# Performance work log

Measured on AMD Instinct MI355X. Metric: run time of the kernel, lower is better.

Reference implementation:

```python
import jax, jax.numpy as jnp
import numpy as np

B, S, D, H = 2, 2048, 1024, 16
DK = D // H


def setup_inputs() -> dict:
    key = jax.random.key(0)
    ks = jax.random.split(key, 12)
    scale = 1.0 / np.sqrt(D)
    return {
        "query": jax.random.normal(ks[0], (B, S, D), jnp.float32),
        "key": jax.random.normal(ks[1], (B, S, D), jnp.float32),
        "value": jax.random.normal(ks[2], (B, S, D), jnp.float32),
        "mask": jax.random.randint(ks[3], (B, S), 0, 2, jnp.int32),
        "Wq": jax.random.normal(ks[4], (D, D), jnp.float32) * scale,
        "bq": jnp.zeros((D,), jnp.float32),
        "Wk": jax.random.normal(ks[5], (D, D), jnp.float32) * scale,
        "bk": jnp.zeros((D,), jnp.float32),
        "Wv": jax.random.normal(ks[6], (D, D), jnp.float32) * scale,
        "bv": jnp.zeros((D,), jnp.float32),
        "Wo": jax.random.normal(ks[7], (D, D), jnp.float32) * scale,
        "bo": jnp.zeros((D,), jnp.float32),
    }


def _proj_split(x, W, b):
    # torch Linear: x @ W.T + b, then [B,S,D] -> [B,H,S,DK]
    y = x @ W.T + b
    return y.reshape(B, S, H, DK).transpose(0, 2, 1, 3)


def reference(query, key, value, mask, Wq, bq, Wk, bk, Wv, bv, Wo, bo):
    q = _proj_split(query, Wq, bq)  # [B,H,S,DK]
    k = _proj_split(key, Wk, bk)
    v = _proj_split(value, Wv, bv)
    scores = jnp.einsum("bhqd,bhkd->bhqk", q, k) / jnp.sqrt(jnp.float32(DK))
    # 2D mask -> [B,1,1,S], masked_fill(mask==0, -1e9)
    m = mask[:, None, None, :]
    scores = jnp.where(m == 0, jnp.float32(-1e9), scores)
    attn = jax.nn.softmax(scores, axis=-1)  # dropout p=0.0 -> identity
    x = jnp.einsum("bhqk,bhkd->bhqd", attn, v)
    x = x.transpose(0, 2, 1, 3).reshape(B, S, D)
    output = x @ Wo.T + bo
    return output, attn
```

## Files before the change

kernel.cpp:

```cpp
#include <hip/hip_runtime.h>
#include <hip/hip_bf16.h>
#include <stdint.h>

typedef __bf16 bf16;
typedef __bf16 bf16x8 __attribute__((ext_vector_type(8)));
typedef float f32x4 __attribute__((ext_vector_type(4)));

#define MFMA16(a, b, c) __builtin_amdgcn_mfma_f32_16x16x32_bf16((a), (b), (c), 0, 0, 0)

__device__ __forceinline__ void g2lds16(const void* g, void* l) {
  __builtin_amdgcn_global_load_lds((__attribute__((address_space(1))) void*)g,
                                   (__attribute__((address_space(3))) void*)l,
                                   16, 0, 0);
}

__global__ __launch_bounds__(256) void cvt3(const float* __restrict__ a,
                                            const float* __restrict__ b,
                                            const float* __restrict__ c,
                                            bf16* x, bf16* y, bf16* z_) {
  int zi = blockIdx.y;
  const float* s = (zi == 0) ? a : (zi == 1) ? b : c;
  bf16* d = (zi == 0) ? x : (zi == 1) ? y : z_;
  size_t i = ((size_t)blockIdx.x * 256 + threadIdx.x) * 8;
  float4 f0 = *(const float4*)(s + i);
  float4 f1 = *(const float4*)(s + i + 4);
  union { bf16 h[8]; uint4 u; } t;
  t.h[0] = (bf16)f0.x; t.h[1] = (bf16)f0.y; t.h[2] = (bf16)f0.z; t.h[3] = (bf16)f0.w;
  t.h[4] = (bf16)f1.x; t.h[5] = (bf16)f1.y; t.h[6] = (bf16)f1.z; t.h[7] = (bf16)f1.w;
  *(uint4*)(d + i) = t.u;
}
__global__ __launch_bounds__(256) void cvt4(const float* __restrict__ a,
                                            const float* __restrict__ b,
                                            const float* __restrict__ c,
                                            const float* __restrict__ e,
                                            bf16* x, bf16* y, bf16* z_, bf16* w) {
  int zi = blockIdx.y;
  const float* s = (zi == 0) ? a : (zi == 1) ? b : (zi == 2) ? c : e;
  bf16* d = (zi == 0) ? x : (zi == 1) ? y : (zi == 2) ? z_ : w;
  size_t i = ((size_t)blockIdx.x * 256 + threadIdx.x) * 8;
  float4 f0 = *(const float4*)(s + i);
  float4 f1 = *(const float4*)(s + i + 4);
  union { bf16 h[8]; uint4 u; } t;
  t.h[0] = (bf16)f0.x; t.h[1] = (bf16)f0.y; t.h[2] = (bf16)f0.z; t.h[3] = (bf16)f0.w;
  t.h[4] = (bf16)f1.x; t.h[5] = (bf16)f1.y; t.h[6] = (bf16)f1.z; t.h[7] = (bf16)f1.w;
  *(uint4*)(d + i) = t.u;
}

__device__ __forceinline__ void gemm_core_128(const bf16* __restrict__ A,
                                              const bf16* __restrict__ W,
                                              int m0, int n0, int tid,
                                              uint4* sA, uint4* sB,
                                              f32x4 acc[4][4]) {
  const int lane = tid & 63, quad = lane >> 4, l16 = lane & 15;
  const int wave = tid >> 6;
  const int wm = (wave >> 1) * 64, wn = (wave & 1) * 64;
#pragma unroll
  for (int i = 0; i < 4; i++)
#pragma unroll
    for (int j = 0; j < 4; j++) {
      f32x4 z = {0.f, 0.f, 0.f, 0.f};
      acc[i][j] = z;
    }
  for (int kk = 0; kk < 16; kk++) {
    const int k0 = kk * 64;
    __syncthreads();
#pragma unroll
    for (int t = 0; t < 4; t++) {
      int c = t * 256 + tid;
      int r = c >> 3, jb = (c & 7) ^ (r & 7);
      g2lds16(A + (size_t)(m0 + r) * 1024 + k0 + jb * 8, sA + c);
    }
#pragma unroll
    for (int t = 0; t < 4; t++) {
      int c = t * 256 + tid;
      int r = c >> 3, jb = (c & 7) ^ (r & 7);
      g2lds16(W + (size_t)(n0 + r) * 1024 + k0 + jb * 8, sB + c);
    }
    __syncthreads();
#pragma unroll
    for (int kc = 0; kc < 2; kc++) {
      bf16x8 af[4], bfr[4];
#pragma unroll
      for (int i = 0; i < 4; i++) {
        int row = wm + i * 16 + l16;
        af[i] = *(const bf16x8*)(sA + row * 8 + (((kc << 2) + quad) ^ (row & 7)));
      }
#pragma unroll
      for (int j = 0; j < 4; j++) {
        int row = wn + j * 16 + l16;
        bfr[j] = *(const bf16x8*)(sB + row * 8 + (((kc << 2) + quad) ^ (row & 7)));
      }
#pragma unroll
      for (int i = 0; i < 4; i++)
#pragma unroll
        for (int j = 0; j < 4; j++)
          acc[i][j] = MFMA16(af[i], bfr[j], acc[i][j]);
    }
  }
}


__global__ __launch_bounds__(256, 2) void qkv_gemm(
    const bf16* __restrict__ qin, const bf16* __restrict__ kin,
    const bf16* __restrict__ vin, const bf16* __restrict__ Wq,
    const bf16* __restrict__ Wk, const bf16* __restrict__ Wv,
    const float* __restrict__ bq, const float* __restrict__ bk,
    const float* __restrict__ bv, bf16* __restrict__ qw, bf16* __restrict__ kw,
    bf16* __restrict__ vTw) {
  __shared__ uint4 sA[1024], sB[1024];
  const int z = blockIdx.z;
  const bf16* A = (z == 0) ? qin : (z == 1) ? kin : vin;
  const bf16* W = (z == 0) ? Wq : (z == 1) ? Wk : Wv;
  const float* bias = (z == 0) ? bq : (z == 1) ? bk : bv;
  const int m0 = blockIdx.x * 128, n0 = blockIdx.y * 128;
  const int tid = threadIdx.x;
  f32x4 acc[4][4];
  gemm_core_128(A, W, m0, n0, tid, sA, sB, acc);
  const int lane = tid & 63, quad = lane >> 4, l16 = lane & 15;
  const int wave = tid >> 6;
  const int wm = (wave >> 1) * 64, wn = (wave & 1) * 64;
  if (z < 2) {
    bf16* out = (z == 0) ? qw : kw;
#pragma unroll
    for (int j = 0; j < 4; j++) {
      int n = n0 + wn + j * 16 + l16;
      float bvv = bias[n];
      int h = n >> 6, dk = n & 63;
#pragma unroll
      for (int i = 0; i < 4; i++) {
        int mbase = m0 + wm + i * 16 + quad * 4;
#pragma unroll
        for (int r = 0; r < 4; r++) {
          int m = mbase + r;
          int b = m >> 11, s = m & 2047;
          out[(((size_t)(b * 16 + h) * 2048 + s) << 6) + dk] =
              (bf16)(acc[i][j][r] + bvv);
        }
      }
    }
  } else {
#pragma unroll
    for (int j = 0; j < 4; j++) {
      int n = n0 + wn + j * 16 + l16;
      float bvv = bias[n];
      int h = n >> 6, dk = n & 63;
#pragma unroll
      for (int i = 0; i < 4; i++) {
        int m = m0 + wm + i * 16 + quad * 4;
        int b = m >> 11, s = m & 2047;
        union { bf16 hh[4]; uint2 u; } tmp;
#pragma unroll
        for (int r = 0; r < 4; r++) tmp.hh[r] = (bf16)(acc[i][j][r] + bvv);
        *(uint2*)&vTw[((size_t)((b * 16 + h) * 64 + dk) << 11) + s] = tmp.u;
      }
    }
  }
}

__global__ __launch_bounds__(256, 2) void out_gemm(const bf16* __restrict__ X,
                                                   const bf16* __restrict__ Wo,
                                                   const float* __restrict__ bo,
                                                   float* __restrict__ out) {
  __shared__ uint4 sA[1024], sB[1024];
  const int m0 = blockIdx.x * 128, n0 = blockIdx.y * 128;
  const int tid = threadIdx.x;
  f32x4 acc[4][4];
  gemm_core_128(X, Wo, m0, n0, tid, sA, sB, acc);
  const int lane = tid & 63, quad = lane >> 4, l16 = lane & 15;
  const int wave = tid >> 6;
  const int wm = (wave >> 1) * 64, wn = (wave & 1) * 64;
#pragma unroll
  for (int j = 0; j < 4; j++) {
    int n = n0 + wn + j * 16 + l16;
    float bvv = bo[n];
#pragma unroll
    for (int i = 0; i < 4; i++) {
      int mbase = m0 + wm + i * 16 + quad * 4;
#pragma unroll
      for (int r = 0; r < 4; r++) {
        int m = mbase + r;
        out[((size_t)m << 10) + n] = acc[i][j][r] + bvv;
      }
    }
  }
}

__global__ __launch_bounds__(256, 2) void attn_kernel(
    const bf16* __restrict__ qw, const bf16* __restrict__ kw,
    const bf16* __restrict__ vT, const int* __restrict__ mask,
    float* __restrict__ attnF, bf16* __restrict__ xw) {
  __shared__ uint4 smem[4096];
  uint4* const sK0 = smem;
  uint4* const sK1 = smem + 1024;
  uint4* const sV = smem + 2048;
  uint4* const sP = smem + 3072;
  uint4* const sQ = smem + 3072;

  const int tid = threadIdx.x, wave = tid >> 6, lane = tid & 63;
  const int quad = lane >> 4, l16 = lane & 15;
  const int wgid = blockIdx.y * 32 + blockIdx.x;
  const int swz = (wgid & 7) * 128 + (wgid >> 3);
  const int qt = swz & 31, bh = swz >> 5, b = bh >> 4, h = bh & 15;
  const int q0 = qt * 64;
  const bf16* qbase = qw + (size_t)bh * (2048 * 64);
  const bf16* kbase = kw + (size_t)bh * (2048 * 64);
  const bf16* vbase = vT + (size_t)bh * (64 * 2048);
  const int* mrow = mask + b * 2048;

  auto stageK = [&](uint4* buf, int kt) {
#pragma unroll
    for (int t = 0; t < 4; t++) {
      int c = t * 256 + tid;
      int r = c >> 3, jb = (c & 7) ^ (r & 7);
      g2lds16(kbase + (size_t)(kt * 128 + r) * 64 + jb * 8, buf + c);
    }
  };
  auto stageV = [&](int kt) {
#pragma unroll
    for (int t = 0; t < 4; t++) {
      int c = t * 256 + tid;
      int rv = c >> 4, jb = (c & 15) ^ (rv & 15);
      g2lds16(vbase + (size_t)rv * 2048 + kt * 128 + jb * 8, sV + c);
    }
  };

#pragma unroll
  for (int t = 0; t < 2; t++) {
    int c = t * 256 + tid;
    int r = c >> 3, jb = (c & 7) ^ (r & 7);
    g2lds16(qbase + (size_t)(q0 + r) * 64 + jb * 8, sQ + c);
  }
  stageK(sK0, 0);
  __syncthreads();

  bf16x8 aq[2];
  {
    int row = wave * 16 + l16;
    aq[0] = *(const bf16x8*)(sQ + row * 8 + ((quad) ^ (row & 7)));
    aq[1] = *(const bf16x8*)(sQ + row * 8 + ((4 + quad) ^ (row & 7)));
  }
  float lrun[4];
#pragma unroll
  for (int r = 0; r < 4; r++) lrun[r] = 0.f;

  for (int kt = 0; kt < 16; kt++) {
    uint4* kcur = (kt & 1) ? sK1 : sK0;
    if (kt < 15) {
      stageK((kt & 1) ? sK0 : sK1, kt + 1);
    } else {
      stageK(sK0, 0);
      stageV(0);
    }
    f32x4 sc[8];
#pragma unroll
    for (int ns = 0; ns < 8; ns++) {
      f32x4 z = {0.f, 0.f, 0.f, 0.f};
      sc[ns] = z;
    }
#pragma unroll
    for (int kc = 0; kc < 2; kc++)
#pragma unroll
      for (int ns = 0; ns < 8; ns++) {
        int row = ns * 16 + l16;
        bf16x8 bk =
            *(const bf16x8*)(kcur + row * 8 + (((kc << 2) + quad) ^ (row & 7)));
        sc[ns] = MFMA16(aq[kc], bk, sc[ns]);
      }
    float psum[4];
#pragma unroll
    for (int r = 0; r < 4; r++) psum[r] = 0.f;
#pragma unroll
    for (int ns = 0; ns < 8; ns++) {
      float madd = (mrow[kt * 128 + ns * 16 + l16] == 0) ? -1.0e9f : 0.0f;
#pragma unroll
      for (int r = 0; r < 4; r++)
        psum[r] += __expf(sc[ns][r] * 0.125f + madd);
    }
#pragma unroll
    for (int r = 0; r < 4; r++) {
#pragma unroll
      for (int off = 8; off >= 1; off >>= 1)
        psum[r] += __shfl_xor(psum[r], off, 16);
      lrun[r] += psum[r];
    }
    __syncthreads();
  }

  float invl[4];
  size_t arow[4];
#pragma unroll
  for (int r = 0; r < 4; r++) {
    invl[r] = 1.f / fmaxf(lrun[r], 1.0e-30f);
    arow[r] = (size_t)(bh * 2048 + q0 + wave * 16 + quad * 4 + r) * 2048;
  }
  f32x4 xacc[4];
#pragma unroll
  for (int nd = 0; nd < 4; nd++) {
    f32x4 z = {0.f, 0.f, 0.f, 0.f};
    xacc[nd] = z;
  }
  bf16* sPb = (bf16*)sP;

  for (int kt = 0; kt < 16; kt++) {
    uint4* kcur = (kt & 1) ? sK1 : sK0;
    if (kt < 15) stageK((kt & 1) ? sK0 : sK1, kt + 1);
    f32x4 sc[8];
#pragma unroll
    for (int ns = 0; ns < 8; ns++) {
      f32x4 z = {0.f, 0.f, 0.f, 0.f};
      sc[ns] = z;
    }
#pragma unroll
    for (int kc = 0; kc < 2; kc++)
#pragma unroll
      for (int ns = 0; ns < 8; ns++) {
        int row = ns * 16 + l16;
        bf16x8 bk =
            *(const bf16x8*)(kcur + row * 8 + (((kc << 2) + quad) ^ (row & 7)));
        sc[ns] = MFMA16(aq[kc], bk, sc[ns]);
      }
#pragma unroll
    for (int ns = 0; ns < 8; ns++) {
      float madd = (mrow[kt * 128 + ns * 16 + l16] == 0) ? -1.0e9f : 0.0f;
      int col = ns * 16 + l16;
#pragma unroll
      for (int r = 0; r < 4; r++) {
        float p = __expf(sc[ns][r] * 0.125f + madd) * invl[r];
        sc[ns][r] = p;
        int qrow = wave * 16 + quad * 4 + r;
        int chunk = qrow * 16 + ((col >> 3) ^ (qrow & 15));
        sPb[chunk * 8 + (col & 7)] = (bf16)p;
      }
    }
    __syncthreads();
#pragma unroll
    for (int kc2 = 0; kc2 < 4; kc2++) {
      int rowp = wave * 16 + l16;
      bf16x8 ap =
          *(const bf16x8*)(sP + rowp * 16 + (((kc2 << 2) + quad) ^ (rowp & 15)));
#pragma unroll
      for (int nd = 0; nd < 4; nd++) {
        int rv = nd * 16 + l16;
        bf16x8 bv =
            *(const bf16x8*)(sV + rv * 16 + (((kc2 << 2) + quad) ^ (rv & 15)));
        xacc[nd] = MFMA16(ap, bv, xacc[nd]);
      }
    }
    __syncthreads();
    if (kt < 15) stageV(kt + 1);
#pragma unroll
    for (int ns = 0; ns < 8; ns++) {
      int col = kt * 128 + ns * 16 + l16;
#pragma unroll
      for (int r = 0; r < 4; r++)
        __builtin_nontemporal_store(sc[ns][r], &attnF[arow[r] + col]);
    }
  }
#pragma unroll
  for (int nd = 0; nd < 4; nd++) {
    int dk = nd * 16 + l16;
#pragma unroll
    for (int r = 0; r < 4; r++) {
      int qrow = q0 + wave * 16 + quad * 4 + r;
      xw[((size_t)(b * 2048 + qrow) << 10) + h * 64 + dk] = (bf16)xacc[nd][r];
    }
  }
}

extern "C" void kernel_launch(void* const* d_in, const int* in_sizes, int n_in,
                              void* d_out, int out_size, void* d_ws,
                              size_t ws_size, hipStream_t stream) {
  const float* query = (const float*)d_in[0];
  const float* key = (const float*)d_in[1];
  const float* value = (const float*)d_in[2];
  const int* mask = (const int*)d_in[3];
  const float* Wq = (const float*)d_in[4];
  const float* bq = (const float*)d_in[5];
  const float* Wk = (const float*)d_in[6];
  const float* bk = (const float*)d_in[7];
  const float* Wv = (const float*)d_in[8];
  const float* bv = (const float*)d_in[9];
  const float* Wo = (const float*)d_in[10];
  const float* bo = (const float*)d_in[11];

  float* outF = (float*)d_out;
  float* attnF = outF + (size_t)4194304;

  bf16* tQ = (bf16*)attnF;
  bf16* tK = tQ + (size_t)4194304;
  bf16* tV = tK + (size_t)4194304;
  bf16* tWq = tV + (size_t)4194304;
  bf16* tWk = tWq + (size_t)1048576;
  bf16* tWv = tWk + (size_t)1048576;

  bf16* qw = (bf16*)d_ws;
  bf16* kw = qw + (size_t)4194304;
  bf16* vT = kw + (size_t)4194304;
  bf16* xw = vT + (size_t)4194304;
  bf16* WoB = xw + (size_t)4194304;

  cvt3<<<dim3(2048, 3), 256, 0, stream>>>(query, key, value, tQ, tK, tV);
  cvt4<<<dim3(512, 4), 256, 0, stream>>>(Wq, Wk, Wv, Wo, tWq, tWk, tWv, WoB);
  qkv_gemm<<<dim3(32, 8, 3), 256, 0, stream>>>(tQ, tK, tV, tWq, tWk, tWv, bq,
                                               bk, bv, qw, kw, vT);
  attn_kernel<<<dim3(32, 32), 256, 0, stream>>>(qw, kw, vT, mask, attnF, xw);
  out_gemm<<<dim3(32, 8), 256, 0, stream>>>(xw, WoB, bo, outF);
}
```

Baseline: 725.0 us.

## Load K/V directly from global memory and drop LDS staging in attention

Removes the double-buffered LDS staging of K, V and Q in the attention kernel. MFMA operands are now read straight from global memory, relying on L1/L2 caching since the four waves share K/V tiles. The smaller LDS footprint allows the launch bound to rise to 4 blocks per CU for more occupancy, and the attention-probability stores move inside the exp loop. The cost is uncoalesced global reads (V rows strided by 2048) with no asynchronous prefetch, and repeated cache traffic in place of LDS reuse.

After: 920.9 us. +27.0%, slower.

```diff
diff --git a/kernel.cpp b/kernel.cpp
--- a/kernel.cpp
+++ b/kernel.cpp
@@ -185,16 +185,11 @@
   }
 }
 
-__global__ __launch_bounds__(256, 2) void attn_kernel(
+__global__ __launch_bounds__(256, 4) void attn_kernel(
     const bf16* __restrict__ qw, const bf16* __restrict__ kw,
     const bf16* __restrict__ vT, const int* __restrict__ mask,
     float* __restrict__ attnF, bf16* __restrict__ xw) {
-  __shared__ uint4 smem[4096];
-  uint4* const sK0 = smem;
-  uint4* const sK1 = smem + 1024;
-  uint4* const sV = smem + 2048;
-  uint4* const sP = smem + 3072;
-  uint4* const sQ = smem + 3072;
+  __shared__ uint4 sP[1024];
 
   const int tid = threadIdx.x, wave = tid >> 6, lane = tid & 63;
   const int quad = lane >> 4, l16 = lane & 15;
@@ -207,50 +202,18 @@
   const bf16* vbase = vT + (size_t)bh * (64 * 2048);
   const int* mrow = mask + b * 2048;
 
-  auto stageK = [&](uint4* buf, int kt) {
-#pragma unroll
-    for (int t = 0; t < 4; t++) {
-      int c = t * 256 + tid;
-      int r = c >> 3, jb = (c & 7) ^ (r & 7);
-      g2lds16(kbase + (size_t)(kt * 128 + r) * 64 + jb * 8, buf + c);
-    }
-  };
-  auto stageV = [&](int kt) {
-#pragma unroll
-    for (int t = 0; t < 4; t++) {
-      int c = t * 256 + tid;
-      int rv = c >> 4, jb = (c & 15) ^ (rv & 15);
-      g2lds16(vbase + (size_t)rv * 2048 + kt * 128 + jb * 8, sV + c);
-    }
-  };
-
-#pragma unroll
-  for (int t = 0; t < 2; t++) {
-    int c = t * 256 + tid;
-    int r = c >> 3, jb = (c & 7) ^ (r & 7);
-    g2lds16(qbase + (size_t)(q0 + r) * 64 + jb * 8, sQ + c);
-  }
-  stageK(sK0, 0);
-  __syncthreads();
-
   bf16x8 aq[2];
   {
-    int row = wave * 16 + l16;
-    aq[0] = *(const bf16x8*)(sQ + row * 8 + ((quad) ^ (row & 7)));
-    aq[1] = *(const bf16x8*)(sQ + row * 8 + ((4 + quad) ^ (row & 7)));
+    const bf16* qrow_p = qbase + (size_t)(q0 + wave * 16 + l16) * 64;
+    aq[0] = *(const bf16x8*)(qrow_p + quad * 8);
+    aq[1] = *(const bf16x8*)(qrow_p + 32 + quad * 8);
   }
   float lrun[4];
 #pragma unroll
   for (int r = 0; r < 4; r++) lrun[r] = 0.f;
 
   for (int kt = 0; kt < 16; kt++) {
-    uint4* kcur = (kt & 1) ? sK1 : sK0;
-    if (kt < 15) {
-      stageK((kt & 1) ? sK0 : sK1, kt + 1);
-    } else {
-      stageK(sK0, 0);
-      stageV(0);
-    }
+    const bf16* ktb = kbase + (size_t)kt * 128 * 64;
     f32x4 sc[8];
 #pragma unroll
     for (int ns = 0; ns < 8; ns++) {
@@ -261,9 +224,8 @@
     for (int kc = 0; kc < 2; kc++)
 #pragma unroll
       for (int ns = 0; ns < 8; ns++) {
-        int row = ns * 16 + l16;
-        bf16x8 bk =
-            *(const bf16x8*)(kcur + row * 8 + (((kc << 2) + quad) ^ (row & 7)));
+        bf16x8 bk = *(const bf16x8*)(ktb + (size_t)(ns * 16 + l16) * 64 +
+                                     kc * 32 + quad * 8);
         sc[ns] = MFMA16(aq[kc], bk, sc[ns]);
       }
     float psum[4];
@@ -283,7 +245,6 @@
         psum[r] += __shfl_xor(psum[r], off, 16);
       lrun[r] += psum[r];
     }
-    __syncthreads();
   }
 
   float invl[4];
@@ -302,8 +263,7 @@
   bf16* sPb = (bf16*)sP;
 
   for (int kt = 0; kt < 16; kt++) {
-    uint4* kcur = (kt & 1) ? sK1 : sK0;
-    if (kt < 15) stageK((kt & 1) ? sK0 : sK1, kt + 1);
+    const bf16* ktb = kbase + (size_t)kt * 128 * 64;
     f32x4 sc[8];
 #pragma unroll
     for (int ns = 0; ns < 8; ns++) {
@@ -314,9 +274,8 @@
     for (int kc = 0; kc < 2; kc++)
 #pragma unroll
       for (int ns = 0; ns < 8; ns++) {
-        int row = ns * 16 + l16;
-        bf16x8 bk =
-            *(const bf16x8*)(kcur + row * 8 + (((kc << 2) + quad) ^ (row & 7)));
+        bf16x8 bk = *(const bf16x8*)(ktb + (size_t)(ns * 16 + l16) * 64 +
+                                     kc * 32 + quad * 8);
         sc[ns] = MFMA16(aq[kc], bk, sc[ns]);
       }
 #pragma unroll
@@ -326,10 +285,10 @@
 #pragma unroll
       for (int r = 0; r < 4; r++) {
         float p = __expf(sc[ns][r] * 0.125f + madd) * invl[r];
-        sc[ns][r] = p;
         int qrow = wave * 16 + quad * 4 + r;
         int chunk = qrow * 16 + ((col >> 3) ^ (qrow & 15));
         sPb[chunk * 8 + (col & 7)] = (bf16)p;
+        __builtin_nontemporal_store(p, &attnF[arow[r] + kt * 128 + col]);
       }
     }
     __syncthreads();
@@ -340,21 +299,12 @@
           *(const bf16x8*)(sP + rowp * 16 + (((kc2 << 2) + quad) ^ (rowp & 15)));
 #pragma unroll
       for (int nd = 0; nd < 4; nd++) {
-        int rv = nd * 16 + l16;
-        bf16x8 bv =
-            *(const bf16x8*)(sV + rv * 16 + (((kc2 << 2) + quad) ^ (rv & 15)));
+        bf16x8 bv = *(const bf16x8*)(vbase + (size_t)(nd * 16 + l16) * 2048 +
+                                     kt * 128 + kc2 * 32 + quad * 8);
         xacc[nd] = MFMA16(ap, bv, xacc[nd]);
       }
     }
     __syncthreads();
-    if (kt < 15) stageV(kt + 1);
-#pragma unroll
-    for (int ns = 0; ns < 8; ns++) {
-      int col = kt * 128 + ns * 16 + l16;
-#pragma unroll
-      for (int r = 0; r < 4; r++)
-        __builtin_nontemporal_store(sc[ns][r], &attnF[arow[r] + col]);
-    }
   }
 #pragma unroll
   for (int nd = 0; nd < 4; nd++) {
```
